# Kernel tuning notes

Hardware: AMD Instinct MI355X
Metric: run time of the kernel (lower is better)

Reference implementation:

```python
import jax, jax.numpy as jnp
import numpy as np

N_NODES = 50000
N_EDGES = 800000
F_IN = 128
HID = 128
N_CLS = 10


def _gcn_conv(x, src, dst, n, W, b):
    # PyG GCNConv: h = x @ W, symmetric normalization with self-loops, scatter-add, + bias
    h = x @ W                                   # [N, H]
    deg = jax.ops.segment_sum(jnp.ones_like(dst, dtype=x.dtype), dst, num_segments=n)
    dinv = jnp.where(deg > 0, jax.lax.rsqrt(deg), 0.0)  # deg includes self-loops
    w = dinv[src] * dinv[dst]                   # [E+N]
    agg = jax.ops.segment_sum(h[src] * w[:, None], dst, num_segments=n)  # [N, H]
    return agg + b


def reference(x, edge_index, W1, b1, Ws1, bs1, W2, b2, Ws2, bs2, Wc, bc):
    n = x.shape[0]
    loops = jnp.arange(n, dtype=edge_index.dtype)
    src = jnp.concatenate([edge_index[0], loops])  # add self-loops
    dst = jnp.concatenate([edge_index[1], loops])

    x = jax.nn.relu(_gcn_conv(x, src, dst, n, W1, b1) + x @ Ws1 + bs1)
    x = jax.nn.relu(_gcn_conv(x, src, dst, n, W2, b2) + x @ Ws2 + bs2)

    x_avg = jnp.mean(x, axis=0, keepdims=True)  # [1, H]
    return x_avg @ Wc + bc                      # [1, C]


def setup_inputs() -> dict:
    key = jax.random.key(0)
    ks = jax.random.split(key, 12)
    s = 0.05
    return {
        "x": jax.random.normal(ks[0], (N_NODES, F_IN), jnp.float32),
        "edge_index": jax.random.randint(ks[1], (2, N_EDGES), 0, N_NODES, dtype=jnp.int64),
        "W1": jax.random.normal(ks[2], (F_IN, HID), jnp.float32) * s,
        "b1": jnp.zeros((HID,), jnp.float32),
        "Ws1": jax.random.normal(ks[3], (F_IN, HID), jnp.float32) * s,
        "bs1": jnp.zeros((HID,), jnp.float32),
        "W2": jax.random.normal(ks[4], (HID, HID), jnp.float32) * s,
        "b2": jnp.zeros((HID,), jnp.float32),
        "Ws2": jax.random.normal(ks[5], (HID, HID), jnp.float32) * s,
        "bs2": jnp.zeros((HID,), jnp.float32),
        "Wc": jax.random.normal(ks[6], (HID, N_CLS), jnp.float32) * s,
        "bc": jnp.zeros((N_CLS,), jnp.float32),
    }
```

## Files before the change

### kernel.cpp

```cpp
#include <hip/hip_runtime.h>

#define FEAT 128
#define N_CLS 10

typedef unsigned int uint;
typedef __attribute__((ext_vector_type(8))) short short8v;
typedef __attribute__((ext_vector_type(4))) float f32x4;

__device__ inline unsigned short f2bf(float f) {
    union { float f; uint u; } c; c.f = f;
    uint r = (c.u + 0x7FFFu + ((c.u >> 16) & 1u)) >> 16;
    return (unsigned short)r;
}
__device__ inline float bfhi(uint u) {
    union { uint u; float f; } c; c.u = u & 0xFFFF0000u;
    return c.f;
}
__device__ inline float bflo(uint u) {
    union { uint u; float f; } c; c.u = u << 16;
    return c.f;
}

__global__ void k_init(int* deg, float* colsum, int n) {
    int i = blockIdx.x * blockDim.x + threadIdx.x;
    if (i < n) deg[i] = 0;
    if (i < FEAT) colsum[i] = 0.f;
}

__global__ void k_hist(const int* __restrict__ dst, int* deg,
                       unsigned short* __restrict__ rank, int E) {
    int e = blockIdx.x * blockDim.x + threadIdx.x;
    if (e < E) {
        int r = atomicAdd(&deg[dst[e]], 1);
        rank[e] = (unsigned short)r;
    }
}

__global__ __launch_bounds__(256) void k_bsum(const int* __restrict__ deg,
                                              int* __restrict__ bsum, int n) {
    int i = blockIdx.x * 256 + threadIdx.x;
    int v = (i < n) ? deg[i] : 0;
    #pragma unroll
    for (int d = 32; d; d >>= 1) v += __shfl_down(v, d, 64);
    __shared__ int ws[4];
    int lane = threadIdx.x & 63, wid = threadIdx.x >> 6;
    if (lane == 0) ws[wid] = v;
    __syncthreads();
    if (threadIdx.x == 0) bsum[blockIdx.x] = ws[0] + ws[1] + ws[2] + ws[3];
}

__global__ __launch_bounds__(256) void k_bscan(int* bsum, int nb) {
    __shared__ int lds[256];
    int t = threadIdx.x;
    int v = (t < nb) ? bsum[t] : 0;
    lds[t] = v;
    __syncthreads();
    #pragma unroll
    for (int d = 1; d < 256; d <<= 1) {
        int u = (t >= d) ? lds[t - d] : 0;
        __syncthreads();
        lds[t] += u;
        __syncthreads();
    }
    if (t < nb) bsum[t] = lds[t] - v;
}

__global__ __launch_bounds__(256) void k_write(const int* __restrict__ deg,
                                               const int* __restrict__ bsum,
                                               int* off, float* dinv,
                                               int n, int E) {
    __shared__ int lds[256];
    int t = threadIdx.x;
    int i = blockIdx.x * 256 + t;
    int v = (i < n) ? deg[i] : 0;
    lds[t] = v;
    __syncthreads();
    #pragma unroll
    for (int d = 1; d < 256; d <<= 1) {
        int u = (t >= d) ? lds[t - d] : 0;
        __syncthreads();
        lds[t] += u;
        __syncthreads();
    }
    if (i < n) {
        off[i] = bsum[blockIdx.x] + (lds[t] - v);
        dinv[i] = rsqrtf((float)(deg[i] + 1));
    }
    if (i == n - 1) off[n] = E;
}

__global__ void k_fill(const int* __restrict__ src, const int* __restrict__ dst,
                       const unsigned short* __restrict__ rank,
                       const int* __restrict__ off, int* __restrict__ csr, int E) {
    int e = blockIdx.x * blockDim.x + threadIdx.x;
    if (e < E) {
        int d = dst[e];
        csr[off[d] + (int)rank[e]] = src[e];
    }
}

__global__ __launch_bounds__(256) void k_trans(const float* __restrict__ Wsrc,
                                               unsigned short* __restrict__ Wt) {
    int idx = blockIdx.x * 256 + threadIdx.x;
    int c = idx >> 7, k = idx & 127;
    Wt[c * FEAT + k] = f2bf(Wsrc[k * FEAT + c]);
}

__global__ __launch_bounds__(256) void k_gemm(
    const float* __restrict__ x, const unsigned short* __restrict__ Wt,
    const unsigned short* __restrict__ Wst, const float* __restrict__ b,
    const float* __restrict__ bs, const float* __restrict__ dinv,
    unsigned short* __restrict__ hs, float* __restrict__ xs, int n) {
    __shared__ unsigned short x_lds[64 * 136];
    int tid = threadIdx.x;
    int pair = blockIdx.x >> 1;
    int which = blockIdx.x & 1;
    int row0 = pair * 64;

    int c4 = (tid & 31) * 4;
    int rl = tid >> 5;
    #pragma unroll
    for (int p = 0; p < 8; ++p) {
        int r = rl + p * 8;
        float4 v = make_float4(0.f, 0.f, 0.f, 0.f);
        if (row0 + r < n) v = *(const float4*)&x[(size_t)(row0 + r) * FEAT + c4];
        uint2 pk;
        pk.x = (uint)f2bf(v.x) | ((uint)f2bf(v.y) << 16);
        pk.y = (uint)f2bf(v.z) | ((uint)f2bf(v.w) << 16);
        *(uint2*)&x_lds[r * 136 + c4] = pk;
    }
    __syncthreads();

    int wv = tid >> 6;
    int lane = tid & 63;
    int lr = lane & 15;
    int lg = lane >> 4;

    short8v a[4];
    #pragma unroll
    for (int ks = 0; ks < 4; ++ks)
        a[ks] = *(const short8v*)&x_lds[(wv * 16 + lr) * 136 + ks * 32 + lg * 8];

    const unsigned short* Wp = which ? Wst : Wt;
    f32x4 acc[8];
    #pragma unroll
    for (int ct = 0; ct < 8; ++ct) acc[ct] = (f32x4){0.f, 0.f, 0.f, 0.f};

    #pragma unroll
    for (int ct = 0; ct < 8; ++ct) {
        #pragma unroll
        for (int ks = 0; ks < 4; ++ks) {
            short8v bf = *(const short8v*)&Wp[(size_t)(ct * 16 + lr) * FEAT + ks * 32 + lg * 8];
            acc[ct] = __builtin_amdgcn_mfma_f32_16x16x32_bf16(bf, a[ks], acc[ct], 0, 0, 0);
        }
    }

    int node = row0 + wv * 16 + lr;
    int cb4 = lg * 4;
    if (node < n) {
        if (which == 0) {
            float dv = dinv[node];
            #pragma unroll
            for (int ct = 0; ct < 8; ++ct) {
                int col = ct * 16 + cb4;
                uint2 pk;
                pk.x = (uint)f2bf(acc[ct][0] * dv) | ((uint)f2bf(acc[ct][1] * dv) << 16);
                pk.y = (uint)f2bf(acc[ct][2] * dv) | ((uint)f2bf(acc[ct][3] * dv) << 16);
                *(uint2*)&hs[(size_t)node * FEAT + col] = pk;
            }
        } else {
            #pragma unroll
            for (int ct = 0; ct < 8; ++ct) {
                int col = ct * 16 + cb4;
                float4 bb  = *(const float4*)&b[col];
                float4 bb2 = *(const float4*)&bs[col];
                float4 o = make_float4(acc[ct][0] + bb.x + bb2.x,
                                       acc[ct][1] + bb.y + bb2.y,
                                       acc[ct][2] + bb.z + bb2.z,
                                       acc[ct][3] + bb.w + bb2.w);
                *(float4*)&xs[(size_t)node * FEAT + col] = o;
            }
        }
    }
}

__global__ __launch_bounds__(256) void k_agg(
    const unsigned short* __restrict__ hs, float* __restrict__ xs,
    const float* __restrict__ dinv, const int* __restrict__ off,
    const int* __restrict__ csr, int n) {
    int node = (blockIdx.x * 256 + threadIdx.x) >> 5;
    int sub = threadIdx.x & 31;
    if (node >= n) return;
    size_t fo = (size_t)sub * 4;
    const uint2* hp = (const uint2*)&hs[(size_t)node * FEAT + fo];
    uint2 p = *hp;
    float4 a0 = make_float4(bflo(p.x), bfhi(p.x), bflo(p.y), bfhi(p.y));
    float4 a1 = make_float4(0.f, 0.f, 0.f, 0.f);
    float4 a2 = make_float4(0.f, 0.f, 0.f, 0.f);
    float4 a3 = make_float4(0.f, 0.f, 0.f, 0.f);
    int s = off[node], e = off[node + 1];
    int j = s;
    for (; j + 4 <= e; j += 4) {
        int u0 = csr[j], u1 = csr[j + 1], u2 = csr[j + 2], u3 = csr[j + 3];
        uint2 q0 = *(const uint2*)&hs[(size_t)u0 * FEAT + fo];
        uint2 q1 = *(const uint2*)&hs[(size_t)u1 * FEAT + fo];
        uint2 q2 = *(const uint2*)&hs[(size_t)u2 * FEAT + fo];
        uint2 q3 = *(const uint2*)&hs[(size_t)u3 * FEAT + fo];
        a0.x += bflo(q0.x); a0.y += bfhi(q0.x); a0.z += bflo(q0.y); a0.w += bfhi(q0.y);
        a1.x += bflo(q1.x); a1.y += bfhi(q1.x); a1.z += bflo(q1.y); a1.w += bfhi(q1.y);
        a2.x += bflo(q2.x); a2.y += bfhi(q2.x); a2.z += bflo(q2.y); a2.w += bfhi(q2.y);
        a3.x += bflo(q3.x); a3.y += bfhi(q3.x); a3.z += bflo(q3.y); a3.w += bfhi(q3.y);
    }
    for (; j < e; ++j) {
        int u = csr[j];
        uint2 q = *(const uint2*)&hs[(size_t)u * FEAT + fo];
        a0.x += bflo(q.x); a0.y += bfhi(q.x); a0.z += bflo(q.y); a0.w += bfhi(q.y);
    }
    float4 acc;
    acc.x = (a0.x + a1.x) + (a2.x + a3.x);
    acc.y = (a0.y + a1.y) + (a2.y + a3.y);
    acc.z = (a0.z + a1.z) + (a2.z + a3.z);
    acc.w = (a0.w + a1.w) + (a2.w + a3.w);
    float dv = dinv[node];
    size_t o = (size_t)node * FEAT + fo;
    float4 sk = *(const float4*)&xs[o];
    float4 out;
    out.x = fmaxf(fmaf(acc.x, dv, sk.x), 0.f);
    out.y = fmaxf(fmaf(acc.y, dv, sk.y), 0.f);
    out.z = fmaxf(fmaf(acc.z, dv, sk.z), 0.f);
    out.w = fmaxf(fmaf(acc.w, dv, sk.w), 0.f);
    *(float4*)&xs[o] = out;
}

__global__ __launch_bounds__(256) void k_colsum(const float* __restrict__ x2,
                                                float* colsum, int n) {
    __shared__ float lds[256];
    int tid = threadIdx.x;
    int f = tid & 127;
    int half = tid >> 7;
    float acc = 0.f;
    for (int r = blockIdx.x * 2 + half; r < n; r += gridDim.x * 2)
        acc += x2[(size_t)r * FEAT + f];
    lds[tid] = acc;
    __syncthreads();
    if (tid < 128) atomicAdd(&colsum[f], lds[f] + lds[f + 128]);
}

__global__ void k_final(const float* __restrict__ colsum, const float* __restrict__ Wc,
                        const float* __restrict__ bc, float* out, int n) {
    int c = threadIdx.x;
    if (c < N_CLS) {
        float acc = 0.f;
        for (int f = 0; f < FEAT; ++f) acc += colsum[f] * Wc[f * N_CLS + c];
        out[c] = acc / (float)n + bc[c];
    }
}

extern "C" void kernel_launch(void* const* d_in, const int* in_sizes, int n_in,
                              void* d_out, int out_size, void* d_ws, size_t ws_size,
                              hipStream_t stream) {
    const float* x   = (const float*)d_in[0];
    const int*   ei  = (const int*)d_in[1];
    const float* W1  = (const float*)d_in[2];
    const float* b1  = (const float*)d_in[3];
    const float* Ws1 = (const float*)d_in[4];
    const float* bs1 = (const float*)d_in[5];
    const float* W2  = (const float*)d_in[6];
    const float* b2  = (const float*)d_in[7];
    const float* Ws2 = (const float*)d_in[8];
    const float* bs2 = (const float*)d_in[9];
    const float* Wc  = (const float*)d_in[10];
    const float* bc  = (const float*)d_in[11];
    float* out = (float*)d_out;

    const int n = in_sizes[0] / FEAT;
    const int E = in_sizes[1] / 2;
    const int* src = ei;
    const int* dst = ei + E;

    const int nb = (n + 255) / 256;

    char* w = (char*)d_ws;
    auto alloc = [&](size_t bytes) -> void* {
        void* p = (void*)w;
        w += (bytes + 255) & ~(size_t)255;
        return p;
    };
    int*   deg    = (int*)alloc((size_t)n * 4);
    int*   off    = (int*)alloc(((size_t)n + 1) * 4);
    int*   csr    = (int*)alloc((size_t)E * 4);
    unsigned short* rank = (unsigned short*)alloc((size_t)E * 2);
    float* dinv   = (float*)alloc((size_t)n * 4);
    float* colsum = (float*)alloc(FEAT * 4);
    int*   bsum   = (int*)alloc((size_t)nb * 4);
    unsigned short* Wt1  = (unsigned short*)alloc(FEAT * FEAT * 2);
    unsigned short* Wst1 = (unsigned short*)alloc(FEAT * FEAT * 2);
    unsigned short* Wt2  = (unsigned short*)alloc(FEAT * FEAT * 2);
    unsigned short* Wst2 = (unsigned short*)alloc(FEAT * FEAT * 2);
    unsigned short* A = (unsigned short*)alloc((size_t)n * FEAT * 2);
    float* B = (float*)alloc((size_t)n * FEAT * 4);
    float* C = (float*)alloc((size_t)n * FEAT * 4);

    k_init<<<nb, 256, 0, stream>>>(deg, colsum, n);
    k_hist<<<(E + 255) / 256, 256, 0, stream>>>(dst, deg, rank, E);
    k_bsum<<<nb, 256, 0, stream>>>(deg, bsum, n);
    k_bscan<<<1, 256, 0, stream>>>(bsum, nb);
    k_write<<<nb, 256, 0, stream>>>(deg, bsum, off, dinv, n, E);
    k_fill<<<(E + 255) / 256, 256, 0, stream>>>(src, dst, rank, off, csr, E);

    k_trans<<<64, 256, 0, stream>>>(W1, Wt1);
    k_trans<<<64, 256, 0, stream>>>(Ws1, Wst1);
    k_trans<<<64, 256, 0, stream>>>(W2, Wt2);
    k_trans<<<64, 256, 0, stream>>>(Ws2, Wst2);

    int gemm_grid = 2 * ((n + 63) / 64);
    int agg_grid  = (n + 7) / 8;

    k_gemm<<<gemm_grid, 256, 0, stream>>>(x, Wt1, Wst1, b1, bs1, dinv, A, B, n);
    k_agg<<<agg_grid, 256, 0, stream>>>(A, B, dinv, off, csr, n);
    k_gemm<<<gemm_grid, 256, 0, stream>>>(B, Wt2, Wst2, b2, bs2, dinv, A, C, n);
    k_agg<<<agg_grid, 256, 0, stream>>>(A, C, dinv, off, csr, n);

    k_colsum<<<512, 256, 0, stream>>>(C, colsum, n);
    k_final<<<1, 64, 0, stream>>>(colsum, Wc, bc, out, n);
}
```

Baseline: 342.1 us.

## Preload per-wave weight column tiles into registers and loop over node groups

```diff
diff --git a/kernel.cpp b/kernel.cpp
--- a/kernel.cpp
+++ b/kernel.cpp
@@ -129,56 +129,68 @@
         pk.y = (uint)f2bf(v.z) | ((uint)f2bf(v.w) << 16);
         *(uint2*)&x_lds[r * 136 + c4] = pk;
     }
-    __syncthreads();
 
     int wv = tid >> 6;
     int lane = tid & 63;
     int lr = lane & 15;
     int lg = lane >> 4;
-
-    short8v a[4];
-    #pragma unroll
-    for (int ks = 0; ks < 4; ++ks)
-        a[ks] = *(const short8v*)&x_lds[(wv * 16 + lr) * 136 + ks * 32 + lg * 8];
+    int ctb = wv * 2;
 
     const unsigned short* Wp = which ? Wst : Wt;
-    f32x4 acc[8];
-    #pragma unroll
-    for (int ct = 0; ct < 8; ++ct) acc[ct] = (f32x4){0.f, 0.f, 0.f, 0.f};
-
-    #pragma unroll
-    for (int ct = 0; ct < 8; ++ct) {
+    short8v wf[2][4];
+    #pragma unroll
+    for (int c = 0; c < 2; ++c)
+        #pragma unroll
+        for (int ks = 0; ks < 4; ++ks)
+            wf[c][ks] = *(const short8v*)&Wp[(size_t)((ctb + c) * 16 + lr) * FEAT + ks * 32 + lg * 8];
+
+    float4 bias[2];
+    #pragma unroll
+    for (int c = 0; c < 2; ++c) {
+        int col = (ctb + c) * 16 + lg * 4;
+        float4 bb  = *(const float4*)&b[col];
+        float4 bb2 = *(const float4*)&bs[col];
+        bias[c] = make_float4(bb.x + bb2.x, bb.y + bb2.y, bb.z + bb2.z, bb.w + bb2.w);
+    }
+
+    __syncthreads();
+
+    #pragma unroll
+    for (int ng = 0; ng < 4; ++ng) {
+        short8v a[4];
+        #pragma unroll
+        for (int ks = 0; ks < 4; ++ks)
+            a[ks] = *(const short8v*)&x_lds[(ng * 16 + lr) * 136 + ks * 32 + lg * 8];
+
+        f32x4 acc[2];
+        acc[0] = (f32x4){0.f, 0.f, 0.f, 0.f};
+        acc[1] = (f32x4){0.f, 0.f, 0.f, 0.f};
         #pragma unroll
         for (int ks = 0; ks < 4; ++ks) {
-            short8v bf = *(const short8v*)&Wp[(size_t)(ct * 16 + lr) * FEAT + ks * 32 + lg * 8];
-            acc[ct] = __builtin_amdgcn_mfma_f32_16x16x32_bf16(bf, a[ks], acc[ct], 0, 0, 0);
+            acc[0] = __builtin_amdgcn_mfma_f32_16x16x32_bf16(wf[0][ks], a[ks], acc[0], 0, 0, 0);
+            acc[1] = __builtin_amdgcn_mfma_f32_16x16x32_bf16(wf[1][ks], a[ks], acc[1], 0, 0, 0);
         }
-    }
-
-    int node = row0 + wv * 16 + lr;
-    int cb4 = lg * 4;
-    if (node < n) {
-        if (which == 0) {
-            float dv = dinv[node];
-            #pragma unroll
-            for (int ct = 0; ct < 8; ++ct) {
-                int col = ct * 16 + cb4;
-                uint2 pk;
-                pk.x = (uint)f2bf(acc[ct][0] * dv) | ((uint)f2bf(acc[ct][1] * dv) << 16);
-                pk.y = (uint)f2bf(acc[ct][2] * dv) | ((uint)f2bf(acc[ct][3] * dv) << 16);
-                *(uint2*)&hs[(size_t)node * FEAT + col] = pk;
-            }
-        } else {
-            #pragma unroll
-            for (int ct = 0; ct < 8; ++ct) {
-                int col = ct * 16 + cb4;
-                float4 bb  = *(const float4*)&b[col];
-                float4 bb2 = *(const float4*)&bs[col];
-                float4 o = make_float4(acc[ct][0] + bb.x + bb2.x,
-                                       acc[ct][1] + bb.y + bb2.y,
-                                       acc[ct][2] + bb.z + bb2.z,
-                                       acc[ct][3] + bb.w + bb2.w);
-                *(float4*)&xs[(size_t)node * FEAT + col] = o;
+
+        int node = row0 + ng * 16 + lr;
+        if (node < n) {
+            if (which == 0) {
+                float dv = dinv[node];
+                #pragma unroll
+                for (int c = 0; c < 2; ++c) {
+                    int col = (ctb + c) * 16 + lg * 4;
+                    uint2 pk;
+                    pk.x = (uint)f2bf(acc[c][0] * dv) | ((uint)f2bf(acc[c][1] * dv) << 16);
+                    pk.y = (uint)f2bf(acc[c][2] * dv) | ((uint)f2bf(acc[c][3] * dv) << 16);
+                    *(uint2*)&hs[(size_t)node * FEAT + col] = pk;
+                }
+            } else {
+                #pragma unroll
+                for (int c = 0; c < 2; ++c) {
+                    int col = (ctb + c) * 16 + lg * 4;
+                    float4 o = make_float4(acc[c][0] + bias[c].x, acc[c][1] + bias[c].y,
+                                           acc[c][2] + bias[c].z, acc[c][3] + bias[c].w);
+                    *(float4*)&xs[(size_t)node * FEAT + col] = o;
+                }
             }
         }
     }
```

After: 296.7 us. 13.3% less time.
